# Performance work log

Measured on AMD Instinct MI355X. Metric: run time of the kernel, lower is better.

The kernel has to match this reference:

```python
import jax, jax.numpy as jnp
import numpy as np

# config (stands in for global `args` in the original repo)
N = 8192            # args.tRNA + args.disease
NNZ = 262144        # number of edges in adj
N_SEEDS = 256
MASK_DEPTH = 2      # args.maskDepth
KEEP_RATE = 0.9     # args.keepRate


def setup_inputs() -> dict:
    rng = np.random.default_rng(0)
    # duplicate-free edge list (coalesced sparse tensor)
    h = rng.choice(N * N, size=NNZ, replace=False)
    adj_rows = jnp.asarray(h // N, dtype=jnp.int32)
    adj_cols = jnp.asarray(h % N, dtype=jnp.int32)
    key = jax.random.key(0)
    k1, k2, k3 = jax.random.split(key, 3)
    adj_values = jax.random.uniform(k1, (NNZ,), dtype=jnp.float32)
    seeds = jax.random.randint(k2, (N_SEEDS,), 0, N, dtype=jnp.int32)
    complemental = jax.random.uniform(k3, (N, N), dtype=jnp.float32)
    return {"adj_rows": adj_rows, "adj_cols": adj_cols, "adj_values": adj_values,
            "seeds": seeds, "complemental": complemental}


def _forward(adj_rows, adj_cols, adj_values, seeds, complemental):
    rows, cols = adj_rows, adj_cols
    # --- BFS edge masking (sequential per-seed removal == union removal) ---
    keep = jnp.ones((NNZ,), bool)
    seed_mask = jnp.zeros((N,), bool).at[seeds].set(True)
    mask_nodes = seed_mask
    for i in range(MASK_DEPTH):
        incident = keep & (seed_mask[rows] | seed_mask[cols])
        keep = keep & ~incident
        if i != MASK_DEPTH - 1:
            inc_i = incident.astype(jnp.int32)
            nxt = (jnp.zeros((N,), jnp.int32).at[rows].add(inc_i)
                   .at[cols].add(inc_i)) > 0
            seed_mask = nxt
            mask_nodes = mask_nodes | nxt
    # --- random node sampling augments the mask set ---
    key = jax.random.key(42)
    k1, k2, k3 = jax.random.split(key, 3)
    samp_num = int(N * KEEP_RATE)
    samped = jax.random.randint(k1, (samp_num,), 0, N)
    mask_nodes = mask_nodes.at[samped].set(True)
    # --- encoder adj: kept edges, values gathered from complemental, D^-1/2 A D^-1/2 ---
    keep_i = keep.astype(jnp.int32)
    enc_cov = (jnp.zeros((N, N), jnp.int32).at[rows, cols].add(keep_i)) > 0
    enc_dense = jnp.where(enc_cov, complemental, 0.0)
    deg = enc_dense.sum(axis=1)
    norm = (deg + 1e-12) ** -0.5
    enc = enc_dense * norm[:, None] * norm[None, :]
    # --- decoder adj: random mask-node pairs (symmetric) + self loops + kept edges ---
    mask_idx = jnp.nonzero(mask_nodes, size=N, fill_value=0)[0]
    tem_num = mask_nodes.sum()
    u1 = jax.random.uniform(k2, (NNZ,))
    u2 = jax.random.uniform(k3, (NNZ,))
    tem_rows = mask_idx[jnp.floor(u1 * tem_num).astype(jnp.int32)]
    tem_cols = mask_idx[jnp.floor(u2 * tem_num).astype(jnp.int32)]
    ar = jnp.arange(N, dtype=jnp.int32)
    new_rows = jnp.concatenate([tem_rows, tem_cols, ar, rows])
    new_cols = jnp.concatenate([tem_cols, tem_rows, ar, cols])
    valid = jnp.concatenate([jnp.ones((2 * NNZ + N,), jnp.int32), keep_i])
    # hash-dedup in the original == coverage set; values depend only on (r,c)
    dec_cov = (jnp.zeros((N, N), jnp.int32).at[new_rows, new_cols].add(valid)) > 0
    dec = jnp.where(dec_cov, complemental, 0.0)
    return enc, dec


def reference(adj_rows, adj_cols, adj_values, seeds, complemental):
    return _forward(adj_rows, adj_cols, adj_values, seeds, complemental)
```

## Files before the change

kernel.cpp:

```cpp
#include <hip/hip_runtime.h>
#include <stdint.h>
#include <math.h>

static __device__ __forceinline__ uint32_t rotl32(uint32_t x, int r) {
    return (x << r) | (x >> (32 - r));
}

static __device__ __forceinline__ void tf2x32(uint32_t k0, uint32_t k1,
                                              uint32_t& x0, uint32_t& x1) {
    uint32_t ks2 = k0 ^ k1 ^ 0x1BD11BDAu;
    x0 += k0; x1 += k1;
#define TFR(r) { x0 += x1; x1 = rotl32(x1, r); x1 ^= x0; }
    TFR(13) TFR(15) TFR(26) TFR(6)
    x0 += k1;  x1 += ks2 + 1u;
    TFR(17) TFR(29) TFR(16) TFR(24)
    x0 += ks2; x1 += k0 + 2u;
    TFR(13) TFR(15) TFR(26) TFR(6)
    x0 += k0;  x1 += k1 + 3u;
    TFR(17) TFR(29) TFR(16) TFR(24)
    x0 += k1;  x1 += ks2 + 4u;
    TFR(13) TFR(15) TFR(26) TFR(6)
    x0 += ks2; x1 += k0 + 5u;
#undef TFR
}

struct SubKeys { uint32_t k1a, k1b, k2a, k2b, k3a, k3b; };

static __device__ __forceinline__ SubKeys derive_keys() {
    uint32_t a0 = 0, b0 = 3; tf2x32(0u, 42u, a0, b0);
    uint32_t a1 = 1, b1 = 4; tf2x32(0u, 42u, a1, b1);
    uint32_t a2 = 2, b2 = 5; tf2x32(0u, 42u, a2, b2);
    SubKeys s; s.k1a = a0; s.k1b = a1; s.k2a = a2; s.k2b = b0; s.k3a = b1; s.k3b = b2;
    return s;
}

static __device__ __forceinline__ float bits_to_unit_float(uint32_t b) {
    return __uint_as_float((b >> 9) | 0x3f800000u) - 1.0f;
}

__global__ void k_seed(const int* __restrict__ seeds, int n_seeds,
                       unsigned char* __restrict__ seedm) {
    int i = blockIdx.x * blockDim.x + threadIdx.x;
    if (i < n_seeds) seedm[seeds[i]] = 1;
}

__global__ void k_edge1(const int* __restrict__ rows, const int* __restrict__ cols, int nnz,
                        const unsigned char* __restrict__ seedm,
                        unsigned char* __restrict__ keep, unsigned char* __restrict__ nxt) {
    int e = blockIdx.x * blockDim.x + threadIdx.x;
    if (e >= nnz) return;
    int r = rows[e], c = cols[e];
    bool inc = (seedm[r] | seedm[c]) != 0;
    keep[e] = inc ? 0 : 1;
    if (inc) { nxt[r] = 1; nxt[c] = 1; }
}

__global__ void k_edge2(const int* __restrict__ rows, const int* __restrict__ cols, int nnz,
                        const unsigned char* __restrict__ nxt,
                        unsigned char* __restrict__ keep) {
    int e = blockIdx.x * blockDim.x + threadIdx.x;
    if (e >= nnz) return;
    if (keep[e] && ((nxt[rows[e]] | nxt[cols[e]]) != 0)) keep[e] = 0;
}

__global__ void k_union(int n, const unsigned char* __restrict__ seedm,
                        const unsigned char* __restrict__ nxt,
                        unsigned char* __restrict__ mask) {
    int i = blockIdx.x * blockDim.x + threadIdx.x;
    if (i < n) mask[i] = (unsigned char)(seedm[i] | nxt[i]);
}

__global__ void k_samp(int half, int modmask, unsigned char* __restrict__ mask) {
    int t = blockIdx.x * blockDim.x + threadIdx.x;
    if (t >= half) return;
    SubKeys sk = derive_keys();
    uint32_t x0 = (uint32_t)t, x1 = (uint32_t)(t + half);
    tf2x32(sk.k1a, sk.k1b, x0, x1);
    mask[x0 & (uint32_t)modmask] = 1;
    mask[x1 & (uint32_t)modmask] = 1;
}

__global__ void __launch_bounds__(1024)
k_scan(int n, const unsigned char* __restrict__ mask,
       int* __restrict__ mask_idx, int* __restrict__ tem_num) {
    __shared__ int ssum[1024];
    int t = threadIdx.x;
    int per = n / 1024;
    int base = t * per;
    int loc[8];
    int s = 0;
    for (int j = 0; j < per; ++j) { loc[j] = mask[base + j]; s += loc[j]; }
    ssum[t] = s;
    __syncthreads();
    for (int off = 1; off < 1024; off <<= 1) {
        int v = (t >= off) ? ssum[t - off] : 0;
        __syncthreads();
        ssum[t] += v;
        __syncthreads();
    }
    int excl = ssum[t] - s;
    for (int j = 0; j < per; ++j)
        if (loc[j]) mask_idx[excl++] = base + j;
    if (t == 1023) *tem_num = ssum[1023];
}

__global__ void k_deg(const int* __restrict__ rows, const int* __restrict__ cols, int nnz,
                      const unsigned char* __restrict__ keep,
                      const float* __restrict__ comp, float* __restrict__ deg, int n) {
    int e = blockIdx.x * blockDim.x + threadIdx.x;
    if (e >= nnz) return;
    if (keep[e]) {
        int r = rows[e], c = cols[e];
        atomicAdd(&deg[r], comp[(size_t)r * n + c]);
    }
}

__global__ void k_norm(int n, const float* __restrict__ deg, float* __restrict__ nrm) {
    int i = blockIdx.x * blockDim.x + threadIdx.x;
    if (i < n) nrm[i] = 1.0f / sqrtf(deg[i] + 1e-12f);
}

__global__ void k_enc(const int* __restrict__ rows, const int* __restrict__ cols, int nnz,
                      const unsigned char* __restrict__ keep,
                      const float* __restrict__ comp, const float* __restrict__ nrm,
                      float* __restrict__ enc, int n) {
    int e = blockIdx.x * blockDim.x + threadIdx.x;
    if (e >= nnz) return;
    if (keep[e]) {
        int r = rows[e], c = cols[e];
        size_t o = (size_t)r * n + c;
        enc[o] = comp[o] * nrm[r] * nrm[c];
    }
}

__global__ void k_dec_base(const int* __restrict__ rows, const int* __restrict__ cols,
                           int nnz, int n, const unsigned char* __restrict__ keep,
                           const float* __restrict__ comp, float* __restrict__ dec) {
    int e = blockIdx.x * blockDim.x + threadIdx.x;
    if (e < nnz) {
        if (keep[e]) {
            size_t o = (size_t)rows[e] * n + cols[e];
            dec[o] = comp[o];
        }
    } else if (e < nnz + n) {
        int i = e - nnz;
        size_t o = (size_t)i * n + i;
        dec[o] = comp[o];
    }
}

__global__ void k_dec_tem(int half, int n, const int* __restrict__ mask_idx,
                          const int* __restrict__ tem_num,
                          const float* __restrict__ comp, float* __restrict__ dec) {
    int e = blockIdx.x * blockDim.x + threadIdx.x;
    if (e >= half) return;
    SubKeys sk = derive_keys();
    float tf = (float)(*tem_num);
    uint32_t u1a = (uint32_t)e, u1b = (uint32_t)(e + half);
    tf2x32(sk.k2a, sk.k2b, u1a, u1b);
    uint32_t u2a = (uint32_t)e, u2b = (uint32_t)(e + half);
    tf2x32(sk.k3a, sk.k3b, u2a, u2b);
#pragma unroll
    for (int j = 0; j < 2; ++j) {
        uint32_t b1 = j ? u1b : u1a;
        uint32_t b2 = j ? u2b : u2a;
        float uu1 = bits_to_unit_float(b1);
        float uu2 = bits_to_unit_float(b2);
        int i1 = (int)(uu1 * tf);
        int i2 = (int)(uu2 * tf);
        int r = mask_idx[i1];
        int c = mask_idx[i2];
        size_t o1 = (size_t)r * n + c;
        size_t o2 = (size_t)c * n + r;
        dec[o1] = comp[o1];
        dec[o2] = comp[o2];
    }
}

extern "C" void kernel_launch(void* const* d_in, const int* in_sizes, int n_in,
                              void* d_out, int out_size, void* d_ws, size_t ws_size,
                              hipStream_t stream) {
    const int*   rows  = (const int*)d_in[0];
    const int*   cols  = (const int*)d_in[1];
    const int*   seeds = (const int*)d_in[3];
    const float* comp  = (const float*)d_in[4];

    const int nnz     = in_sizes[0];
    const int n_seeds = in_sizes[3];
    const int n       = (int)(sqrt((double)in_sizes[4]) + 0.5);

    float* enc = (float*)d_out;
    float* dec = enc + (size_t)n * n;

    char* ws = (char*)d_ws;
    float* deg            = (float*)(ws);
    float* nrm            = (float*)(ws + 4 * (size_t)n);
    int*   mask_idx       = (int*)  (ws + 8 * (size_t)n);
    int*   tem_num        = (int*)  (ws + 12 * (size_t)n);
    unsigned char* seedm  = (unsigned char*)(ws + 12 * (size_t)n + 256);
    unsigned char* nxt    = seedm + n;
    unsigned char* mask   = nxt + n;
    unsigned char* keep   = mask + n;

    size_t zbytes = 12 * (size_t)n + 256 + 3 * (size_t)n;
    hipMemsetAsync(d_ws, 0, zbytes, stream);
    hipMemsetAsync(d_out, 0, (size_t)out_size * sizeof(float), stream);

    const int B = 256;
    k_seed <<<(n_seeds + B - 1) / B, B, 0, stream>>>(seeds, n_seeds, seedm);
    k_edge1<<<(nnz + B - 1) / B, B, 0, stream>>>(rows, cols, nnz, seedm, keep, nxt);
    k_edge2<<<(nnz + B - 1) / B, B, 0, stream>>>(rows, cols, nnz, nxt, keep);
    k_union<<<(n + B - 1) / B, B, 0, stream>>>(n, seedm, nxt, mask);

    int samp_num = (int)((double)n * 0.9);
    int shalf = samp_num / 2;
    k_samp <<<(shalf + B - 1) / B, B, 0, stream>>>(shalf, n - 1, mask);

    k_scan <<<1, 1024, 0, stream>>>(n, mask, mask_idx, tem_num);

    k_deg  <<<(nnz + B - 1) / B, B, 0, stream>>>(rows, cols, nnz, keep, comp, deg, n);
    k_norm <<<(n + B - 1) / B, B, 0, stream>>>(n, deg, nrm);
    k_enc  <<<(nnz + B - 1) / B, B, 0, stream>>>(rows, cols, nnz, keep, comp, nrm, enc, n);

    k_dec_base<<<(nnz + n + B - 1) / B, B, 0, stream>>>(rows, cols, nnz, n, keep, comp, dec);

    int ehalf = nnz / 2;
    k_dec_tem<<<(ehalf + B - 1) / B, B, 0, stream>>>(ehalf, n, mask_idx, tem_num, comp, dec);
}
```

Baseline: 700.3 us.

## Fuse edge masking, output zeroing, degree and decoder passes into fewer kernels

Merges the chain of small kernels into five launches: output zeroing is folded into the first edge pass via a grid-stride float4 fill, the second masking pass also accumulates degree and writes kept decoder entries, and sampling, normalisation and diagonal writes share one kernel. Encoder writes and random decoder pairs share a final kernel. The workspace memset shrinks to the seed and next-frontier flags. This removes launch overhead and the separate 512MB memset, but the zero fill now runs on only 2048 blocks inside a kernel, which may reach lower bandwidth than the driver memset.

```diff
diff --git a/kernel.cpp b/kernel.cpp
--- a/kernel.cpp
+++ b/kernel.cpp
@@ -44,40 +44,67 @@
     if (i < n_seeds) seedm[seeds[i]] = 1;
 }
 
-__global__ void k_edge1(const int* __restrict__ rows, const int* __restrict__ cols, int nnz,
-                        const unsigned char* __restrict__ seedm,
-                        unsigned char* __restrict__ keep, unsigned char* __restrict__ nxt) {
-    int e = blockIdx.x * blockDim.x + threadIdx.x;
-    if (e >= nnz) return;
-    int r = rows[e], c = cols[e];
-    bool inc = (seedm[r] | seedm[c]) != 0;
-    keep[e] = inc ? 0 : 1;
-    if (inc) { nxt[r] = 1; nxt[c] = 1; }
-}
-
-__global__ void k_edge2(const int* __restrict__ rows, const int* __restrict__ cols, int nnz,
-                        const unsigned char* __restrict__ nxt,
-                        unsigned char* __restrict__ keep) {
-    int e = blockIdx.x * blockDim.x + threadIdx.x;
-    if (e >= nnz) return;
-    if (keep[e] && ((nxt[rows[e]] | nxt[cols[e]]) != 0)) keep[e] = 0;
-}
-
-__global__ void k_union(int n, const unsigned char* __restrict__ seedm,
-                        const unsigned char* __restrict__ nxt,
-                        unsigned char* __restrict__ mask) {
-    int i = blockIdx.x * blockDim.x + threadIdx.x;
-    if (i < n) mask[i] = (unsigned char)(seedm[i] | nxt[i]);
-}
-
-__global__ void k_samp(int half, int modmask, unsigned char* __restrict__ mask) {
-    int t = blockIdx.x * blockDim.x + threadIdx.x;
-    if (t >= half) return;
-    SubKeys sk = derive_keys();
-    uint32_t x0 = (uint32_t)t, x1 = (uint32_t)(t + half);
-    tf2x32(sk.k1a, sk.k1b, x0, x1);
-    mask[x0 & (uint32_t)modmask] = 1;
-    mask[x1 & (uint32_t)modmask] = 1;
+__global__ void __launch_bounds__(256)
+k_fill_edge1(const int* __restrict__ rows, const int* __restrict__ cols, int nnz,
+             const unsigned char* __restrict__ seedm,
+             unsigned char* __restrict__ keep, unsigned char* __restrict__ nxt,
+             float* __restrict__ out, size_t out_elems,
+             float* __restrict__ deg, int n) {
+    const int tid = blockIdx.x * blockDim.x + threadIdx.x;
+    const int nt  = gridDim.x * blockDim.x;
+    for (int e = tid; e < nnz; e += nt) {
+        int r = rows[e], c = cols[e];
+        bool inc = (seedm[r] | seedm[c]) != 0;
+        keep[e] = inc ? 0 : 1;
+        if (inc) { nxt[r] = 1; nxt[c] = 1; }
+    }
+    const float4 z = make_float4(0.f, 0.f, 0.f, 0.f);
+    float4* p = (float4*)out;
+    const size_t t4 = out_elems / 4;
+    for (size_t i = tid; i < t4; i += (size_t)nt) p[i] = z;
+    for (int i = tid; i < n; i += nt) deg[i] = 0.0f;
+}
+
+__global__ void __launch_bounds__(256)
+k_edge2_deg_dec(const int* __restrict__ rows, const int* __restrict__ cols, int nnz,
+                const unsigned char* __restrict__ seedm,
+                const unsigned char* __restrict__ nxt,
+                unsigned char* __restrict__ keep, unsigned char* __restrict__ mask,
+                const float* __restrict__ comp, float* __restrict__ deg,
+                float* __restrict__ dec, int n) {
+    const int tid = blockIdx.x * blockDim.x + threadIdx.x;
+    const int nt  = gridDim.x * blockDim.x;
+    for (int e = tid; e < nnz; e += nt) {
+        int r = rows[e], c = cols[e];
+        unsigned char k = keep[e];
+        if (k && ((nxt[r] | nxt[c]) != 0)) { k = 0; keep[e] = 0; }
+        if (k) {
+            size_t o = (size_t)r * n + c;
+            float v = comp[o];
+            atomicAdd(&deg[r], v);
+            dec[o] = v;
+        }
+    }
+    for (int i = tid; i < n; i += nt) mask[i] = (unsigned char)(seedm[i] | nxt[i]);
+}
+
+__global__ void __launch_bounds__(256)
+k_samp_norm_diag(int samp_half, int n, unsigned char* __restrict__ mask,
+                 const float* __restrict__ deg, float* __restrict__ nrm,
+                 const float* __restrict__ comp, float* __restrict__ dec) {
+    const int tid = blockIdx.x * blockDim.x + threadIdx.x;
+    if (tid < samp_half) {
+        SubKeys sk = derive_keys();
+        uint32_t x0 = (uint32_t)tid, x1 = (uint32_t)(tid + samp_half);
+        tf2x32(sk.k1a, sk.k1b, x0, x1);
+        mask[x0 & (uint32_t)(n - 1)] = 1;
+        mask[x1 & (uint32_t)(n - 1)] = 1;
+    }
+    if (tid < n) {
+        nrm[tid] = 1.0f / sqrtf(deg[tid] + 1e-12f);
+        size_t o = (size_t)tid * n + tid;
+        dec[o] = comp[o];
+    }
 }
 
 __global__ void __launch_bounds__(1024)
@@ -104,76 +131,45 @@
     if (t == 1023) *tem_num = ssum[1023];
 }
 
-__global__ void k_deg(const int* __restrict__ rows, const int* __restrict__ cols, int nnz,
-                      const unsigned char* __restrict__ keep,
-                      const float* __restrict__ comp, float* __restrict__ deg, int n) {
-    int e = blockIdx.x * blockDim.x + threadIdx.x;
-    if (e >= nnz) return;
-    if (keep[e]) {
-        int r = rows[e], c = cols[e];
-        atomicAdd(&deg[r], comp[(size_t)r * n + c]);
-    }
-}
-
-__global__ void k_norm(int n, const float* __restrict__ deg, float* __restrict__ nrm) {
-    int i = blockIdx.x * blockDim.x + threadIdx.x;
-    if (i < n) nrm[i] = 1.0f / sqrtf(deg[i] + 1e-12f);
-}
-
-__global__ void k_enc(const int* __restrict__ rows, const int* __restrict__ cols, int nnz,
-                      const unsigned char* __restrict__ keep,
-                      const float* __restrict__ comp, const float* __restrict__ nrm,
-                      float* __restrict__ enc, int n) {
-    int e = blockIdx.x * blockDim.x + threadIdx.x;
-    if (e >= nnz) return;
-    if (keep[e]) {
-        int r = rows[e], c = cols[e];
-        size_t o = (size_t)r * n + c;
-        enc[o] = comp[o] * nrm[r] * nrm[c];
-    }
-}
-
-__global__ void k_dec_base(const int* __restrict__ rows, const int* __restrict__ cols,
-                           int nnz, int n, const unsigned char* __restrict__ keep,
-                           const float* __restrict__ comp, float* __restrict__ dec) {
-    int e = blockIdx.x * blockDim.x + threadIdx.x;
-    if (e < nnz) {
+__global__ void __launch_bounds__(256)
+k_enc_dectem(const int* __restrict__ rows, const int* __restrict__ cols, int nnz,
+             const unsigned char* __restrict__ keep,
+             const float* __restrict__ comp, const float* __restrict__ nrm,
+             float* __restrict__ enc, float* __restrict__ dec,
+             const int* __restrict__ mask_idx, const int* __restrict__ tem_num,
+             int n) {
+    const int tid = blockIdx.x * blockDim.x + threadIdx.x;
+    const int nt  = gridDim.x * blockDim.x;
+    for (int e = tid; e < nnz; e += nt) {
         if (keep[e]) {
-            size_t o = (size_t)rows[e] * n + cols[e];
-            dec[o] = comp[o];
+            int r = rows[e], c = cols[e];
+            size_t o = (size_t)r * n + c;
+            enc[o] = comp[o] * nrm[r] * nrm[c];
         }
-    } else if (e < nnz + n) {
-        int i = e - nnz;
-        size_t o = (size_t)i * n + i;
-        dec[o] = comp[o];
-    }
-}
-
-__global__ void k_dec_tem(int half, int n, const int* __restrict__ mask_idx,
-                          const int* __restrict__ tem_num,
-                          const float* __restrict__ comp, float* __restrict__ dec) {
-    int e = blockIdx.x * blockDim.x + threadIdx.x;
-    if (e >= half) return;
+    }
+    const int ehalf = nnz / 2;
+    const float tf = (float)(*tem_num);
     SubKeys sk = derive_keys();
-    float tf = (float)(*tem_num);
-    uint32_t u1a = (uint32_t)e, u1b = (uint32_t)(e + half);
-    tf2x32(sk.k2a, sk.k2b, u1a, u1b);
-    uint32_t u2a = (uint32_t)e, u2b = (uint32_t)(e + half);
-    tf2x32(sk.k3a, sk.k3b, u2a, u2b);
+    for (int e = tid; e < ehalf; e += nt) {
+        uint32_t u1a = (uint32_t)e, u1b = (uint32_t)(e + ehalf);
+        tf2x32(sk.k2a, sk.k2b, u1a, u1b);
+        uint32_t u2a = (uint32_t)e, u2b = (uint32_t)(e + ehalf);
+        tf2x32(sk.k3a, sk.k3b, u2a, u2b);
 #pragma unroll
-    for (int j = 0; j < 2; ++j) {
-        uint32_t b1 = j ? u1b : u1a;
-        uint32_t b2 = j ? u2b : u2a;
-        float uu1 = bits_to_unit_float(b1);
-        float uu2 = bits_to_unit_float(b2);
-        int i1 = (int)(uu1 * tf);
-        int i2 = (int)(uu2 * tf);
-        int r = mask_idx[i1];
-        int c = mask_idx[i2];
-        size_t o1 = (size_t)r * n + c;
-        size_t o2 = (size_t)c * n + r;
-        dec[o1] = comp[o1];
-        dec[o2] = comp[o2];
+        for (int j = 0; j < 2; ++j) {
+            uint32_t b1 = j ? u1b : u1a;
+            uint32_t b2 = j ? u2b : u2a;
+            float uu1 = bits_to_unit_float(b1);
+            float uu2 = bits_to_unit_float(b2);
+            int i1 = (int)(uu1 * tf);
+            int i2 = (int)(uu2 * tf);
+            int r = mask_idx[i1];
+            int c = mask_idx[i2];
+            size_t o1 = (size_t)r * n + c;
+            size_t o2 = (size_t)c * n + r;
+            dec[o1] = comp[o1];
+            dec[o2] = comp[o2];
+        }
     }
 }
 
@@ -193,37 +189,34 @@
     float* dec = enc + (size_t)n * n;
 
     char* ws = (char*)d_ws;
-    float* deg            = (float*)(ws);
-    float* nrm            = (float*)(ws + 4 * (size_t)n);
-    int*   mask_idx       = (int*)  (ws + 8 * (size_t)n);
-    int*   tem_num        = (int*)  (ws + 12 * (size_t)n);
-    unsigned char* seedm  = (unsigned char*)(ws + 12 * (size_t)n + 256);
-    unsigned char* nxt    = seedm + n;
-    unsigned char* mask   = nxt + n;
-    unsigned char* keep   = mask + n;
-
-    size_t zbytes = 12 * (size_t)n + 256 + 3 * (size_t)n;
-    hipMemsetAsync(d_ws, 0, zbytes, stream);
-    hipMemsetAsync(d_out, 0, (size_t)out_size * sizeof(float), stream);
+    unsigned char* seedm = (unsigned char*)ws;
+    unsigned char* nxt   = seedm + n;
+    unsigned char* mask  = nxt + n;
+    unsigned char* keep  = mask + n;
+    char* ws2 = ws + 3 * (size_t)n + (size_t)nnz;
+    float* deg      = (float*)ws2;
+    float* nrm      = (float*)(ws2 + 4 * (size_t)n);
+    int*   mask_idx = (int*)  (ws2 + 8 * (size_t)n);
+    int*   tem_num  = (int*)  (ws2 + 12 * (size_t)n);
+
+    hipMemsetAsync(ws, 0, 2 * (size_t)n, stream);
 
     const int B = 256;
-    k_seed <<<(n_seeds + B - 1) / B, B, 0, stream>>>(seeds, n_seeds, seedm);
-    k_edge1<<<(nnz + B - 1) / B, B, 0, stream>>>(rows, cols, nnz, seedm, keep, nxt);
-    k_edge2<<<(nnz + B - 1) / B, B, 0, stream>>>(rows, cols, nnz, nxt, keep);
-    k_union<<<(n + B - 1) / B, B, 0, stream>>>(n, seedm, nxt, mask);
-
-    int samp_num = (int)((double)n * 0.9);
-    int shalf = samp_num / 2;
-    k_samp <<<(shalf + B - 1) / B, B, 0, stream>>>(shalf, n - 1, mask);
-
-    k_scan <<<1, 1024, 0, stream>>>(n, mask, mask_idx, tem_num);
-
-    k_deg  <<<(nnz + B - 1) / B, B, 0, stream>>>(rows, cols, nnz, keep, comp, deg, n);
-    k_norm <<<(n + B - 1) / B, B, 0, stream>>>(n, deg, nrm);
-    k_enc  <<<(nnz + B - 1) / B, B, 0, stream>>>(rows, cols, nnz, keep, comp, nrm, enc, n);
-
-    k_dec_base<<<(nnz + n + B - 1) / B, B, 0, stream>>>(rows, cols, nnz, n, keep, comp, dec);
-
-    int ehalf = nnz / 2;
-    k_dec_tem<<<(ehalf + B - 1) / B, B, 0, stream>>>(ehalf, n, mask_idx, tem_num, comp, dec);
-}
+    k_seed<<<(n_seeds + B - 1) / B, B, 0, stream>>>(seeds, n_seeds, seedm);
+
+    k_fill_edge1<<<2048, B, 0, stream>>>(rows, cols, nnz, seedm, keep, nxt,
+                                         enc, (size_t)2 * n * n, deg, n);
+
+    k_edge2_deg_dec<<<(nnz + B - 1) / B, B, 0, stream>>>(rows, cols, nnz, seedm, nxt,
+                                                         keep, mask, comp, deg, dec, n);
+
+    int samp_num  = (int)((double)n * 0.9);
+    int samp_half = samp_num / 2;
+    k_samp_norm_diag<<<(n + B - 1) / B, B, 0, stream>>>(samp_half, n, mask,
+                                                        deg, nrm, comp, dec);
+
+    k_scan<<<1, 1024, 0, stream>>>(n, mask, mask_idx, tem_num);
+
+    k_enc_dectem<<<(nnz + B - 1) / B, B, 0, stream>>>(rows, cols, nnz, keep, comp, nrm,
+                                                      enc, dec, mask_idx, tem_num, n);
+}
```

After: 731.6 us. 1.04x slower.
